# Kernel optimization log

Measured on AMD Instinct MI355X. Metric: run time of the kernel, lower is better.

The kernel has to match this reference:

```python
import jax, jax.numpy as jnp
import numpy as np

B, S, H, NH = 4, 2048, 256, 8
EPS = 1e-5


def setup_inputs() -> dict:
    key = jax.random.key(0)
    ks = jax.random.split(key, 12)
    p = lambda k, shape: (jax.random.normal(k, shape, jnp.float32) * 0.02)
    return {
        "x": jax.random.normal(ks[0], (B, S, H), jnp.float32),
        "lengths": jax.random.randint(ks[1], (B,), 0, S).astype(jnp.int32),
        "atten_in": jnp.zeros((1,), jnp.float32),
        "Wq": p(ks[2], (H, H)), "bq": jnp.zeros((H,), jnp.float32),
        "Wk": p(ks[3], (H, H)), "bk": jnp.zeros((H,), jnp.float32),
        "Wv": p(ks[4], (H, H)), "bv": jnp.zeros((H,), jnp.float32),
        "W1": p(ks[5], (H, H)), "b1": jnp.zeros((H,), jnp.float32),
        "W2": p(ks[6], (H, H)), "b2": jnp.zeros((H,), jnp.float32),
        "g1": jnp.ones((H,), jnp.float32), "beta1": jnp.zeros((H,), jnp.float32),
        "g2": jnp.ones((H,), jnp.float32), "beta2": jnp.zeros((H,), jnp.float32),
    }


def _layer_norm(x, g, b):
    mu = x.mean(-1, keepdims=True)
    var = ((x - mu) ** 2).mean(-1, keepdims=True)
    return (x - mu) / jnp.sqrt(var + EPS) * g + b


def reference(x, lengths, atten_in, Wq, bq, Wk, bk, Wv, bv, W1, b1, W2, b2, g1, beta1, g2, beta2):
    Bx, Sx, Hx = x.shape
    hd = Hx // NH
    # QKV projections, split heads -> [B, NH, S, hd]
    q = (x @ Wq + bq).reshape(Bx, Sx, NH, hd).transpose(0, 2, 1, 3)
    k = (x @ Wk + bk).reshape(Bx, Sx, NH, hd).transpose(0, 2, 1, 3)
    v = (x @ Wv + bv).reshape(Bx, Sx, NH, hd).transpose(0, 2, 1, 3)
    # NOTE: original scales by sqrt(hidden_size), not sqrt(head_dim)
    scores = jnp.einsum('bhqd,bhkd->bhqk', q, k) / np.sqrt(Hx).astype(np.float32)
    pos = jnp.arange(Sx)
    causal = pos[:, None] >= pos[None, :]                     # [S, S]
    row_ok = pos[None, :] < lengths[:, None]                  # [B, S]: mask query rows >= length
    head_ok = jnp.arange(NH)[None, :] < lengths[:, None]      # [B, NH]: original loop masks heads >= length
    mask = causal[None, None] & row_ok[:, None, :, None] & head_ok[:, :, None, None]
    neg = jnp.finfo(scores.dtype).min
    logits = jnp.where(mask, scores, neg)
    atten = jax.nn.softmax(logits, axis=-1)
    # original: masked_fill((atten > 0) == False, 0) -> fully masked rows (NaN in torch) become 0
    atten = jnp.where(mask, atten, 0.0)
    row_valid = mask.any(-1, keepdims=True)
    atten = jnp.where(row_valid, atten, 0.0)
    out = jnp.einsum('bhqk,bhkd->bhqd', atten, v).transpose(0, 2, 1, 3).reshape(Bx, Sx, Hx)
    atten_mean = atten.mean(axis=1)  # [B, S, S], detached in original
    out_1 = x + out  # dropout p=0 / eval mode -> identity
    out_1_norm = _layer_norm(out_1, g1, beta1)
    ff = jax.nn.gelu(out_1_norm @ W1 + b1, approximate=False) @ W2 + b2
    y_prim = _layer_norm(out_1_norm + ff, g2, beta2)
    return (y_prim, lengths, atten_mean)
```

## Files before the change

kernel.cpp:

```cpp
#include <hip/hip_runtime.h>
#include <math.h>

#define BB 4
#define SS 2048
#define HH 256
#define NHH 8
#define EPSV 1e-5f
#define NC 8
#define CHW (SS/NC)
#define NCO 4
#define QPRE 0.09016844005556021f

#if __has_builtin(__builtin_amdgcn_exp2f)
#define EXP2F(x) __builtin_amdgcn_exp2f(x)
#else
#define EXP2F(x) __expf((x) * 0.6931471805599453f)
#endif

typedef unsigned short ushortT;
typedef __attribute__((ext_vector_type(8))) short bf16x8;
typedef __attribute__((ext_vector_type(4))) float f32x4;

__device__ inline ushortT f2bf(float f) {
    union { float f; unsigned int u; } x; x.f = f;
    unsigned int r = x.u + 0x7FFFu + ((x.u >> 16) & 1u);
    return (ushortT)(r >> 16);
}
__device__ inline ushortT f2bf_rz(float f) {
    union { float f; unsigned int u; } x; x.f = f;
    return (ushortT)(x.u >> 16);
}
__device__ inline float bf2f(ushortT u) {
    union { unsigned int i; float f; } x; x.i = ((unsigned int)u) << 16;
    return x.f;
}

__global__ __launch_bounds__(256) void prep(const float* __restrict__ x,
        ushortT* __restrict__ xb, const int* __restrict__ L,
        float* __restrict__ out_len,
        const float* __restrict__ Wa, const float* __restrict__ Wb,
        const float* __restrict__ Wc, const float* __restrict__ Wd,
        const float* __restrict__ We, ushortT* __restrict__ Wtb) {
    const int bid = blockIdx.x;
    if (bid < 1024) {
        const int i = (bid * 256 + threadIdx.x) << 3;
        float4 v0 = *(const float4*)(x + i);
        float4 v1 = *(const float4*)(x + i + 4);
        bf16x8 o;
        o[0] = (short)f2bf(v0.x); o[1] = (short)f2bf(v0.y);
        o[2] = (short)f2bf(v0.z); o[3] = (short)f2bf(v0.w);
        o[4] = (short)f2bf(v1.x); o[5] = (short)f2bf(v1.y);
        o[6] = (short)f2bf(v1.z); o[7] = (short)f2bf(v1.w);
        *(bf16x8*)(xb + i) = o;
        if (bid == 0 && threadIdx.x < BB) out_len[threadIdx.x] = (float)L[threadIdx.x];
        return;
    }
    const int wb = bid - 1024;
    const int z = wb >> 6;
    const int rem = wb & 63;
    const int k0 = (rem >> 3) << 5, n0 = (rem & 7) << 5;
    const float* W = (z == 0) ? Wa : (z == 1) ? Wb : (z == 2) ? Wc : (z == 3) ? Wd : We;
    __shared__ float tile[32][33];
    const int t = threadIdx.x;
    const int r = t >> 3, c4 = (t & 7) << 2;
    float4 v = *(const float4*)(W + (size_t)(k0 + r) * HH + n0 + c4);
    tile[r][c4+0] = v.x; tile[r][c4+1] = v.y; tile[r][c4+2] = v.z; tile[r][c4+3] = v.w;
    __syncthreads();
    ushort4 o;
    o.x = f2bf(tile[c4+0][r]); o.y = f2bf(tile[c4+1][r]);
    o.z = f2bf(tile[c4+2][r]); o.w = f2bf(tile[c4+3][r]);
    *(ushort4*)(Wtb + (size_t)z * 65536 + (size_t)(n0 + r) * HH + k0 + c4) = o;
}

__global__ __launch_bounds__(256) void gemm_qkv(const ushortT* __restrict__ A,
        const ushortT* __restrict__ Wtb,
        const float* __restrict__ bq, const float* __restrict__ bk,
        const float* __restrict__ bv,
        ushortT* __restrict__ Qb, ushortT* __restrict__ Kb,
        ushortT* __restrict__ Vt) {
    __shared__ ushortT As[64][264];
    __shared__ ushortT Ws[64][264];
    const int wsel = blockIdx.y >> 2;
    const int n0 = (blockIdx.y & 3) << 6;
    const ushortT* Wt = Wtb + (size_t)wsel * 65536;
    const float* bias = (wsel == 0) ? bq : (wsel == 1) ? bk : bv;
    const int tid = threadIdx.x;
    const int m0 = blockIdx.x << 6;
    #pragma unroll
    for (int t = 0; t < 8; ++t) {
        const int f = t * 256 + tid;
        const int r = f >> 5;
        const int cc = (f & 31) << 3;
        *(bf16x8*)&As[r][cc] = *(const bf16x8*)(A + (size_t)(m0 + r) * HH + cc);
        *(bf16x8*)&Ws[r][cc] = *(const bf16x8*)(Wt + (size_t)(n0 + r) * HH + cc);
    }
    __syncthreads();
    const int w = tid >> 6, lane = tid & 63;
    const int lg = lane >> 4, lc = lane & 15;
    const int wr = (w & 1) << 5, wc = (w >> 1) << 5;
    f32x4 acc[2][2];
    const f32x4 z4 = {0.f, 0.f, 0.f, 0.f};
    acc[0][0] = z4; acc[0][1] = z4; acc[1][0] = z4; acc[1][1] = z4;
    #pragma unroll
    for (int k0 = 0; k0 < 256; k0 += 32) {
        bf16x8 a0 = *(const bf16x8*)&As[wr + lc][k0 + lg*8];
        bf16x8 a1 = *(const bf16x8*)&As[wr + 16 + lc][k0 + lg*8];
        bf16x8 b0 = *(const bf16x8*)&Ws[wc + lc][k0 + lg*8];
        bf16x8 b1 = *(const bf16x8*)&Ws[wc + 16 + lc][k0 + lg*8];
        acc[0][0] = __builtin_amdgcn_mfma_f32_16x16x32_bf16(a0, b0, acc[0][0], 0, 0, 0);
        acc[0][1] = __builtin_amdgcn_mfma_f32_16x16x32_bf16(a0, b1, acc[0][1], 0, 0, 0);
        acc[1][0] = __builtin_amdgcn_mfma_f32_16x16x32_bf16(a1, b0, acc[1][0], 0, 0, 0);
        acc[1][1] = __builtin_amdgcn_mfma_f32_16x16x32_bf16(a1, b1, acc[1][1], 0, 0, 0);
    }
    ushortT* Out = (wsel == 0) ? Qb : Kb;
    #pragma unroll
    for (int RH = 0; RH < 2; ++RH)
        #pragma unroll
        for (int CH = 0; CH < 2; ++CH) {
            const int col = n0 + wc + CH*16 + lc;
            const float bvv = bias[col];
            float v[4];
            #pragma unroll
            for (int r = 0; r < 4; ++r) {
                v[r] = acc[RH][CH][r] + bvv;
                if (wsel == 0) v[r] *= QPRE;
            }
            if (wsel < 2) {
                #pragma unroll
                for (int r = 0; r < 4; ++r) {
                    const int row = m0 + wr + RH*16 + lg*4 + r;
                    Out[(size_t)row * HH + col] = f2bf(v[r]);
                }
            } else {
                const int row0 = m0 + wr + RH*16 + lg*4;
                const int bidx = row0 >> 11, s0 = row0 & (SS - 1);
                ushort4 o;
                o.x = f2bf(v[0]); o.y = f2bf(v[1]); o.z = f2bf(v[2]); o.w = f2bf(v[3]);
                *(ushort4*)(Vt + ((size_t)(bidx * HH + col)) * SS + s0) = o;
            }
        }
}

template<int MODE>
__global__ __launch_bounds__(256) void gemm_mfma(const ushortT* __restrict__ A,
        const ushortT* __restrict__ Wt, const float* __restrict__ bias,
        void* __restrict__ Cv) {
    __shared__ ushortT As[64][264];
    __shared__ ushortT Ws[64][264];
    const int tid = threadIdx.x;
    const int m0 = blockIdx.x << 6;
    const int n0 = blockIdx.y << 6;
    #pragma unroll
    for (int t = 0; t < 8; ++t) {
        const int f = t * 256 + tid;
        const int r = f >> 5;
        const int cc = (f & 31) << 3;
        *(bf16x8*)&As[r][cc] = *(const bf16x8*)(A + (size_t)(m0 + r) * HH + cc);
        *(bf16x8*)&Ws[r][cc] = *(const bf16x8*)(Wt + (size_t)(n0 + r) * HH + cc);
    }
    __syncthreads();
    const int w = tid >> 6, lane = tid & 63;
    const int lg = lane >> 4, lc = lane & 15;
    const int wr = (w & 1) << 5, wc = (w >> 1) << 5;
    f32x4 acc[2][2];
    const f32x4 z4 = {0.f, 0.f, 0.f, 0.f};
    acc[0][0] = z4; acc[0][1] = z4; acc[1][0] = z4; acc[1][1] = z4;
    #pragma unroll
    for (int k0 = 0; k0 < 256; k0 += 32) {
        bf16x8 a0 = *(const bf16x8*)&As[wr + lc][k0 + lg*8];
        bf16x8 a1 = *(const bf16x8*)&As[wr + 16 + lc][k0 + lg*8];
        bf16x8 b0 = *(const bf16x8*)&Ws[wc + lc][k0 + lg*8];
        bf16x8 b1 = *(const bf16x8*)&Ws[wc + 16 + lc][k0 + lg*8];
        acc[0][0] = __builtin_amdgcn_mfma_f32_16x16x32_bf16(a0, b0, acc[0][0], 0, 0, 0);
        acc[0][1] = __builtin_amdgcn_mfma_f32_16x16x32_bf16(a0, b1, acc[0][1], 0, 0, 0);
        acc[1][0] = __builtin_amdgcn_mfma_f32_16x16x32_bf16(a1, b0, acc[1][0], 0, 0, 0);
        acc[1][1] = __builtin_amdgcn_mfma_f32_16x16x32_bf16(a1, b1, acc[1][1], 0, 0, 0);
    }
    #pragma unroll
    for (int RH = 0; RH < 2; ++RH)
        #pragma unroll
        for (int CH = 0; CH < 2; ++CH) {
            const int col = n0 + wc + CH*16 + lc;
            const float bv = bias[col];
            #pragma unroll
            for (int r = 0; r < 4; ++r) {
                const int row = m0 + wr + RH*16 + lg*4 + r;
                float v = acc[RH][CH][r] + bv;
                if (MODE == 2) v = 0.5f * v * (1.0f + erff(v * 0.70710678118f));
                if (MODE == 0) ((float*)Cv)[(size_t)row * HH + col] = v;
                else           ((ushortT*)Cv)[(size_t)row * HH + col] = f2bf(v);
            }
        }
}

__global__ __launch_bounds__(512) void attn_sums(const ushortT* __restrict__ Qb,
        const ushortT* __restrict__ Kb, const int* __restrict__ lengths,
        float* __restrict__ Psum) {
    const int b = blockIdx.z, c = blockIdx.y;
    const int i0 = (63 - blockIdx.x) << 5;
    const int len = lengths[b];
    const int jmax = min(i0 + 31, len - 1);
    const int jstart = c * CHW;
    if (i0 >= len || jstart > jmax) return;
    const int tid = threadIdx.x;
    const int w = tid >> 6, lane = tid & 63;
    const int lg = lane >> 4, lc = lane & 15;
    bf16x8 qf[2];
    #pragma unroll
    for (int RH = 0; RH < 2; ++RH)
        qf[RH] = *(const bf16x8*)(Qb + ((size_t)(b * SS + i0 + RH*16 + lc)) * HH + w*32 + lg*8);
    const f32x4 z4 = {0.f, 0.f, 0.f, 0.f};
    float lsum[2][4] = {};
    const int jend = min(jstart + CHW - 32, (jmax >> 5) << 5);
    bf16x8 kf0 = *(const bf16x8*)(Kb + ((size_t)(b * SS + jstart + lc)) * HH + w*32 + lg*8);
    bf16x8 kf1 = *(const bf16x8*)(Kb + ((size_t)(b * SS + jstart + 16 + lc)) * HH + w*32 + lg*8);
    for (int j0 = jstart; j0 <= jend; j0 += 32) {
        bf16x8 ck0 = kf0, ck1 = kf1;
        if (j0 + 32 <= jend) {
            kf0 = *(const bf16x8*)(Kb + ((size_t)(b * SS + j0 + 32 + lc)) * HH + w*32 + lg*8);
            kf1 = *(const bf16x8*)(Kb + ((size_t)(b * SS + j0 + 48 + lc)) * HH + w*32 + lg*8);
        }
        f32x4 s[2][2];
        #pragma unroll
        for (int RH = 0; RH < 2; ++RH) {
            s[RH][0] = __builtin_amdgcn_mfma_f32_16x16x32_bf16(qf[RH], ck0, z4, 0, 0, 0);
            s[RH][1] = __builtin_amdgcn_mfma_f32_16x16x32_bf16(qf[RH], ck1, z4, 0, 0, 0);
        }
        if (j0 < i0) {
            #pragma unroll
            for (int RH = 0; RH < 2; ++RH)
                #pragma unroll
                for (int r = 0; r < 4; ++r)
                    #pragma unroll
                    for (int CH = 0; CH < 2; ++CH)
                        lsum[RH][r] += EXP2F(s[RH][CH][r]);
        } else {
            #pragma unroll
            for (int RH = 0; RH < 2; ++RH)
                #pragma unroll
                for (int r = 0; r < 4; ++r) {
                    const int row = i0 + RH*16 + lg*4 + r;
                    #pragma unroll
                    for (int CH = 0; CH < 2; ++CH) {
                        const int j = j0 + CH*16 + lc;
                        lsum[RH][r] += (j <= row) ? EXP2F(s[RH][CH][r]) : 0.f;
                    }
                }
        }
    }
    #pragma unroll
    for (int RH = 0; RH < 2; ++RH)
        #pragma unroll
        for (int r = 0; r < 4; ++r) {
            float v = lsum[RH][r];
            v += __shfl_xor(v, 1); v += __shfl_xor(v, 2);
            v += __shfl_xor(v, 4); v += __shfl_xor(v, 8);
            if (lc == 0)
                Psum[((size_t)(c * BB + b) * NHH + w) * SS + i0 + RH*16 + lg*4 + r] = v;
        }
}

__global__ __launch_bounds__(512) void attn_pv(const ushortT* __restrict__ Qb,
        const ushortT* __restrict__ Kb, const ushortT* __restrict__ Vt,
        const int* __restrict__ lengths, const float* __restrict__ Psum,
        ushortT* __restrict__ OPart, float* __restrict__ out_mean) {
    __shared__ __align__(16) ushortT Pb[2][NHH][32][40];
    __shared__ float invS[NHH][32];
    const int b = blockIdx.z, cg = blockIdx.y;
    const int i0 = (63 - blockIdx.x) << 5;
    const int len = lengths[b];
    const int tid = threadIdx.x;
    const int mr = tid >> 4, mc = (tid & 15) << 1;
    float* meanrow = out_mean + ((size_t)(b * SS + i0 + mr)) * SS + mc;
    const int T = (i0 < len) ? ((min(i0 + 31, len - 1) >> 5) + 1) : 0;
    for (int t = T + ((cg - T) & (NCO - 1)); t < 64; t += NCO)
        *(float2*)(meanrow + (t << 5)) = make_float2(0.f, 0.f);
    const int q = T >> 2, r = T & (NCO - 1);
    const int t0 = cg * q + min(cg, r);
    const int t1 = t0 + q + (cg < r ? 1 : 0);
    if (t0 >= t1) return;
    if (tid < NHH * 32) {
        const int hh = tid >> 5, row = i0 + (tid & 31);
        float rv = 0.f;
        if (row < len && hh < len) {
            float s = 0.f;
            const int ncv = (row >> 8) + 1;
            for (int c2 = 0; c2 < ncv; ++c2)
                s += Psum[((size_t)(c2 * BB + b) * NHH + hh) * SS + row];
            rv = (s > 0.f) ? 1.0f / s : 0.f;
        }
        invS[hh][tid & 31] = rv;
    }
    __syncthreads();
    const int w = tid >> 6, lane = tid & 63;
    const int lg = lane >> 4, lc = lane & 15;
    bf16x8 qf[2];
    #pragma unroll
    for (int RH = 0; RH < 2; ++RH)
        qf[RH] = *(const bf16x8*)(Qb + ((size_t)(b * SS + i0 + RH*16 + lc)) * HH + w*32 + lg*8);
    float invv[2][4];
    #pragma unroll
    for (int RH = 0; RH < 2; ++RH)
        #pragma unroll
        for (int r2 = 0; r2 < 4; ++r2)
            invv[RH][r2] = invS[w][RH*16 + lg*4 + r2];
    float invh8[NHH];
    #pragma unroll
    for (int hh = 0; hh < NHH; ++hh)
        invh8[hh] = invS[hh][mr] * 0.125f;
    const f32x4 z4 = {0.f, 0.f, 0.f, 0.f};
    f32x4 O[2][2];
    O[0][0] = z4; O[0][1] = z4; O[1][0] = z4; O[1][1] = z4;
    const int jstart = t0 << 5;
    bf16x8 kf0 = *(const bf16x8*)(Kb + ((size_t)(b * SS + jstart + lc)) * HH + w*32 + lg*8);
    bf16x8 kf1 = *(const bf16x8*)(Kb + ((size_t)(b * SS + jstart + 16 + lc)) * HH + w*32 + lg*8);
    bf16x8 vf0 = *(const bf16x8*)(Vt + ((size_t)(b * HH + w*32 + lc)) * SS + jstart + lg*8);
    bf16x8 vf1 = *(const bf16x8*)(Vt + ((size_t)(b * HH + w*32 + 16 + lc)) * SS + jstart + lg*8);
    int par = 0;
    for (int t = t0; t < t1; ++t) {
        const int j0 = t << 5;
        bf16x8 ck0 = kf0, ck1 = kf1, cv0 = vf0, cv1 = vf1;
        if (t + 1 < t1) {
            kf0 = *(const bf16x8*)(Kb + ((size_t)(b * SS + j0 + 32 + lc)) * HH + w*32 + lg*8);
            kf1 = *(const bf16x8*)(Kb + ((size_t)(b * SS + j0 + 48 + lc)) * HH + w*32 + lg*8);
            vf0 = *(const bf16x8*)(Vt + ((size_t)(b * HH + w*32 + lc)) * SS + j0 + 32 + lg*8);
            vf1 = *(const bf16x8*)(Vt + ((size_t)(b * HH + w*32 + 16 + lc)) * SS + j0 + 32 + lg*8);
        }
        f32x4 s[2][2];
        #pragma unroll
        for (int RH = 0; RH < 2; ++RH) {
            s[RH][0] = __builtin_amdgcn_mfma_f32_16x16x32_bf16(qf[RH], ck0, z4, 0, 0, 0);
            s[RH][1] = __builtin_amdgcn_mfma_f32_16x16x32_bf16(qf[RH], ck1, z4, 0, 0, 0);
        }
        if (j0 < i0) {
            #pragma unroll
            for (int RH = 0; RH < 2; ++RH)
                #pragma unroll
                for (int CH = 0; CH < 2; ++CH)
                    #pragma unroll
                    for (int r2 = 0; r2 < 4; ++r2)
                        Pb[par][w][RH*16 + lg*4 + r2][CH*16 + lc] =
                            f2bf_rz(EXP2F(s[RH][CH][r2]));
        } else {
            #pragma unroll
            for (int RH = 0; RH < 2; ++RH)
                #pragma unroll
                for (int CH = 0; CH < 2; ++CH)
                    #pragma unroll
                    for (int r2 = 0; r2 < 4; ++r2) {
                        const int row = i0 + RH*16 + lg*4 + r2;
                        const int j = j0 + CH*16 + lc;
                        Pb[par][w][RH*16 + lg*4 + r2][CH*16 + lc] =
                            (j <= row) ? f2bf_rz(EXP2F(s[RH][CH][r2])) : (ushortT)0;
                    }
        }
        #pragma unroll
        for (int RH = 0; RH < 2; ++RH) {
            bf16x8 pa = *(const bf16x8*)&Pb[par][w][RH*16 + lc][lg*8];
            O[RH][0] = __builtin_amdgcn_mfma_f32_16x16x32_bf16(pa, cv0, O[RH][0], 0, 0, 0);
            O[RH][1] = __builtin_amdgcn_mfma_f32_16x16x32_bf16(pa, cv1, O[RH][1], 0, 0, 0);
        }
        __syncthreads();
        float m0 = 0.f, m1 = 0.f;
        #pragma unroll
        for (int ww = 0; ww < NHH; ++ww) {
            ushort2 t2 = *(const ushort2*)&Pb[par][ww][mr][mc];
            m0 += bf2f(t2.x) * invh8[ww]; m1 += bf2f(t2.y) * invh8[ww];
        }
        *(float2*)(meanrow + j0) = make_float2(m0, m1);
        par ^= 1;
    }
    ushortT* op = OPart + (size_t)cg * ((size_t)BB * SS * HH);
    #pragma unroll
    for (int RH = 0; RH < 2; ++RH)
        #pragma unroll
        for (int DH = 0; DH < 2; ++DH)
            #pragma unroll
            for (int r2 = 0; r2 < 4; ++r2)
                op[((size_t)(b * SS + i0 + RH*16 + lg*4 + r2)) * HH + w*32 + DH*16 + lc] =
                    f2bf(O[RH][DH][r2] * invv[RH][r2]);
}

__global__ __launch_bounds__(256) void add_ln_attn(const float* __restrict__ x,
        const ushortT* __restrict__ OPart, const int* __restrict__ lengths,
        const float* __restrict__ g, const float* __restrict__ beta,
        float* __restrict__ out, ushortT* __restrict__ outb) {
    const int row = blockIdx.x;
    const int c = threadIdx.x;
    const int i = row & (SS - 1);
    const int len = lengths[row >> 11];
    const size_t base = (size_t)row * 256;
    float v = x[base + c];
    if (i < len) {
        const int ncv = min(NCO, (i >> 5) + 1);
        for (int cc = 0; cc < ncv; ++cc)
            v += bf2f(OPart[(size_t)cc * ((size_t)BB * SS * HH) + base + c]);
    }
    __shared__ float red[8];
    float s = v;
    #pragma unroll
    for (int o = 32; o; o >>= 1) s += __shfl_down(s, o, 64);
    const int wid = c >> 6, lane = c & 63;
    if (lane == 0) red[wid] = s;
    __syncthreads();
    float mu = (red[0] + red[1] + red[2] + red[3]) * 0.00390625f;
    float d = v - mu;
    float q = d * d;
    #pragma unroll
    for (int o = 32; o; o >>= 1) q += __shfl_down(q, o, 64);
    if (lane == 0) red[4 + wid] = q;
    __syncthreads();
    float var = (red[4] + red[5] + red[6] + red[7]) * 0.00390625f;
    float res = d * rsqrtf(var + EPSV) * g[c] + beta[c];
    out[base + c] = res;
    outb[base + c] = f2bf(res);
}

__global__ __launch_bounds__(256) void add_ln(const float* __restrict__ A,
        const float* __restrict__ Bv, const float* __restrict__ g,
        const float* __restrict__ beta, float* __restrict__ out) {
    const int row = blockIdx.x;
    const int c = threadIdx.x;
    const size_t base = (size_t)row * 256;
    float v = A[base + c] + Bv[base + c];
    __shared__ float red[8];
    float s = v;
    #pragma unroll
    for (int o = 32; o; o >>= 1) s += __shfl_down(s, o, 64);
    const int wid = c >> 6, lane = c & 63;
    if (lane == 0) red[wid] = s;
    __syncthreads();
    float mu = (red[0] + red[1] + red[2] + red[3]) * 0.00390625f;
    float d = v - mu;
    float q = d * d;
    #pragma unroll
    for (int o = 32; o; o >>= 1) q += __shfl_down(q, o, 64);
    if (lane == 0) red[4 + wid] = q;
    __syncthreads();
    float var = (red[4] + red[5] + red[6] + red[7]) * 0.00390625f;
    out[base + c] = d * rsqrtf(var + EPSV) * g[c] + beta[c];
}

extern "C" void kernel_launch(void* const* d_in, const int* in_sizes, int n_in,
                              void* d_out, int out_size, void* d_ws, size_t ws_size,
                              hipStream_t stream) {
    const float* x   = (const float*)d_in[0];
    const int* lengths = (const int*)d_in[1];
    const float* Wq  = (const float*)d_in[3];
    const float* bq  = (const float*)d_in[4];
    const float* Wk  = (const float*)d_in[5];
    const float* bk  = (const float*)d_in[6];
    const float* Wv  = (const float*)d_in[7];
    const float* bv  = (const float*)d_in[8];
    const float* W1  = (const float*)d_in[9];
    const float* b1  = (const float*)d_in[10];
    const float* W2  = (const float*)d_in[11];
    const float* b2  = (const float*)d_in[12];
    const float* g1  = (const float*)d_in[13];
    const float* be1 = (const float*)d_in[14];
    const float* g2  = (const float*)d_in[15];
    const float* be2 = (const float*)d_in[16];
    float* out = (float*)d_out;
    float* ws  = (float*)d_ws;

    const size_t NELT = (size_t)BB * SS * HH;
    const size_t M1 = 1024 * 1024;

    ushortT* xb  = (ushortT*)ws;
    float*   Psum = ws;
    ushortT* Qbf = (ushortT*)(ws + M1);
    ushortT* Kbf = (ushortT*)(ws + 2 * M1);
    ushortT* Vtb = (ushortT*)(ws + 3 * M1);
    float*   X1N  = ws + 4 * M1;
    ushortT* Wtb = (ushortT*)(ws + 6 * M1);
    ushortT* OPart = (ushortT*)(ws + 7 * M1);
    ushortT* X1Nb = (ushortT*)ws;
    ushortT* F1b  = (ushortT*)(ws + M1);
    float*   F2   = ws + 2 * M1;

    float* out_y    = out;
    float* out_len  = out + NELT;
    float* out_mean = out + NELT + 4;

    prep<<<1344, 256, 0, stream>>>(x, xb, lengths, out_len, Wq, Wk, Wv, W1, W2, Wtb);
    gemm_qkv<<<dim3(128, 12), 256, 0, stream>>>(xb, Wtb, bq, bk, bv, Qbf, Kbf, Vtb);
    attn_sums<<<dim3(64, NC, 4), 512, 0, stream>>>(Qbf, Kbf, lengths, Psum);
    attn_pv<<<dim3(64, NCO, 4), 512, 0, stream>>>(Qbf, Kbf, Vtb, lengths, Psum, OPart, out_mean);
    add_ln_attn<<<8192, 256, 0, stream>>>(x, OPart, lengths, g1, be1, X1N, X1Nb);
    gemm_mfma<2><<<dim3(128, 4), 256, 0, stream>>>(X1Nb, Wtb + 3 * 65536, b1, (void*)F1b);
    gemm_mfma<0><<<dim3(128, 4), 256, 0, stream>>>(F1b,  Wtb + 4 * 65536, b2, (void*)F2);
    add_ln<<<8192, 256, 0, stream>>>(X1N, F2, g2, be2, out_y);
}
```

Measured before the change: 104.4 us.

## Widen attention-mean and output stores in attn_pv via batched tiles and LDS staging

The zero-fill of the masked region of atten_mean becomes contiguous float4 row segments split evenly across the column-group blocks, replacing strided float2 stores. The per-tile mean reduction now runs once per pair of 32-column tiles, so it syncs half as often and writes float4 per thread. The bf16 partial output is staged through LDS and written as 16-byte row-contiguous vectors instead of scattered 2-byte stores. This adds an extra barrier per pair and reuses the Pb buffer for staging, so correctness depends on the parity and sync logic being right.

```diff
diff --git a/kernel.cpp b/kernel.cpp
--- a/kernel.cpp
+++ b/kernel.cpp
@@ -270,11 +270,22 @@
     const int i0 = (63 - blockIdx.x) << 5;
     const int len = lengths[b];
     const int tid = threadIdx.x;
-    const int mr = tid >> 4, mc = (tid & 15) << 1;
-    float* meanrow = out_mean + ((size_t)(b * SS + i0 + mr)) * SS + mc;
+    const int mr = tid >> 4;
+    const int w = tid >> 6, lane = tid & 63;
+    const int lg = lane >> 4, lc = lane & 15;
     const int T = (i0 < len) ? ((min(i0 + 31, len - 1) >> 5) + 1) : 0;
-    for (int t = T + ((cg - T) & (NCO - 1)); t < 64; t += NCO)
-        *(float2*)(meanrow + (t << 5)) = make_float2(0.f, 0.f);
+    {
+        const int zc0 = T << 5;
+        const int zq = (SS - zc0) >> 2;
+        const int c0 = zc0 + cg * zq;
+        const int c1 = c0 + zq;
+        #pragma unroll
+        for (int rr = 0; rr < 4; ++rr) {
+            float* mrow0 = out_mean + ((size_t)(b * SS + i0 + w * 4 + rr)) * SS;
+            for (int cc2 = c0 + (lane << 2); cc2 < c1; cc2 += 256)
+                *(float4*)(mrow0 + cc2) = make_float4(0.f, 0.f, 0.f, 0.f);
+        }
+    }
     const int q = T >> 2, r = T & (NCO - 1);
     const int t0 = cg * q + min(cg, r);
     const int t1 = t0 + q + (cg < r ? 1 : 0);
@@ -292,8 +303,6 @@
         invS[hh][tid & 31] = rv;
     }
     __syncthreads();
-    const int w = tid >> 6, lane = tid & 63;
-    const int lg = lane >> 4, lc = lane & 15;
     bf16x8 qf[2];
     #pragma unroll
     for (int RH = 0; RH < 2; ++RH)
@@ -360,25 +369,49 @@
             O[RH][0] = __builtin_amdgcn_mfma_f32_16x16x32_bf16(pa, cv0, O[RH][0], 0, 0, 0);
             O[RH][1] = __builtin_amdgcn_mfma_f32_16x16x32_bf16(pa, cv1, O[RH][1], 0, 0, 0);
         }
-        __syncthreads();
-        float m0 = 0.f, m1 = 0.f;
-        #pragma unroll
-        for (int ww = 0; ww < NHH; ++ww) {
-            ushort2 t2 = *(const ushort2*)&Pb[par][ww][mr][mc];
-            m0 += bf2f(t2.x) * invh8[ww]; m1 += bf2f(t2.y) * invh8[ww];
-        }
-        *(float2*)(meanrow + j0) = make_float2(m0, m1);
-        par ^= 1;
-    }
+        if (par == 1 || t == t1 - 1) {
+            __syncthreads();
+            const int nc = (par + 1) << 5;
+            const int base = (t - par) << 5;
+            const int cb = (tid & 15) << 2;
+            if (cb < nc) {
+                const int sel = cb >> 5, coff = cb & 31;
+                float m0 = 0.f, m1 = 0.f, m2 = 0.f, m3 = 0.f;
+                #pragma unroll
+                for (int ww = 0; ww < NHH; ++ww) {
+                    ushort4 t4 = *(const ushort4*)&Pb[sel][ww][mr][coff];
+                    m0 += bf2f(t4.x) * invh8[ww];
+                    m1 += bf2f(t4.y) * invh8[ww];
+                    m2 += bf2f(t4.z) * invh8[ww];
+                    m3 += bf2f(t4.w) * invh8[ww];
+                }
+                *(float4*)(out_mean + ((size_t)(b * SS + i0 + mr)) * SS + base + cb)
+                    = make_float4(m0, m1, m2, m3);
+            }
+            __syncthreads();
+            par = 0;
+        } else {
+            par = 1;
+        }
+    }
+    ushortT* OLs = &Pb[0][0][0][0];
+    #pragma unroll
+    for (int RH = 0; RH < 2; ++RH)
+        #pragma unroll
+        for (int DH = 0; DH < 2; ++DH)
+            #pragma unroll
+            for (int r2 = 0; r2 < 4; ++r2)
+                OLs[(RH*16 + lg*4 + r2) * 264 + w*32 + DH*16 + lc] =
+                    f2bf(O[RH][DH][r2] * invv[RH][r2]);
+    __syncthreads();
     ushortT* op = OPart + (size_t)cg * ((size_t)BB * SS * HH);
     #pragma unroll
-    for (int RH = 0; RH < 2; ++RH)
-        #pragma unroll
-        for (int DH = 0; DH < 2; ++DH)
-            #pragma unroll
-            for (int r2 = 0; r2 < 4; ++r2)
-                op[((size_t)(b * SS + i0 + RH*16 + lg*4 + r2)) * HH + w*32 + DH*16 + lc] =
-                    f2bf(O[RH][DH][r2] * invv[RH][r2]);
+    for (int rr = 0; rr < 4; rr += 2) {
+        const int row = w*4 + rr + (lane >> 5);
+        const int c8 = (lane & 31) << 3;
+        *(bf16x8*)(op + ((size_t)(b * SS + i0 + row)) * HH + c8) =
+            *(const bf16x8*)&OLs[row * 264 + c8];
+    }
 }
 
 __global__ __launch_bounds__(256) void add_ln_attn(const float* __restrict__ x,
```

Measured after the change: 110.2 us. 5.6% more time.

## Split attention-mean computation out of attn_pv into a separate kernel

Applied to the files above, without the earlier changes.

Moves the head-averaged attention matrix out of attn_pv into a new attn_mean kernel. attn_mean recomputes QK^T for all heads per 32x32 tile and accumulates normalized exp values in registers. attn_pv no longer needs double-buffered LDS, the per-tile __syncthreads, or the cross-wave mean reduction, and the mean work is spread over more blocks (NC=8 column chunks). The cost is a second full QK^T plus exp pass and an extra kernel launch, and the mean is now computed from fp32 exps rather than bf16-rounded probabilities.

```diff
diff --git a/kernel.cpp b/kernel.cpp
--- a/kernel.cpp
+++ b/kernel.cpp
@@ -260,21 +260,108 @@
         }
 }
 
+__global__ __launch_bounds__(512) void attn_mean(const ushortT* __restrict__ Qb,
+        const ushortT* __restrict__ Kb, const int* __restrict__ lengths,
+        const float* __restrict__ Psum, float* __restrict__ out_mean) {
+    __shared__ float invS[NHH][32];
+    const int b = blockIdx.z, c = blockIdx.y;
+    const int i0 = (63 - blockIdx.x) << 5;
+    const int len = lengths[b];
+    const int tid = threadIdx.x;
+    const int w = tid >> 6, lane = tid & 63;
+    const int lg = lane >> 4, lc = lane & 15;
+    const int T = (i0 < len) ? ((min(i0 + 31, len - 1) >> 5) + 1) : 0;
+    {
+        const int zs = max(T * 32 - c * 256, 0);
+        if (zs < 256) {
+            #pragma unroll
+            for (int rr = 0; rr < 4; ++rr) {
+                float* mrow = out_mean + ((size_t)(b * SS + i0 + w * 4 + rr)) * SS + c * 256;
+                const int col = zs + (lane << 2);
+                if (col < 256)
+                    *(float4*)(mrow + col) = make_float4(0.f, 0.f, 0.f, 0.f);
+            }
+        }
+    }
+    if (c * 8 >= T) return;
+    if (tid < NHH * 32) {
+        const int hh = tid >> 5, row = i0 + (tid & 31);
+        float rv = 0.f;
+        if (row < len && hh < len) {
+            float s = 0.f;
+            const int ncv = (row >> 8) + 1;
+            for (int c2 = 0; c2 < ncv; ++c2)
+                s += Psum[((size_t)(c2 * BB + b) * NHH + hh) * SS + row];
+            rv = (s > 0.f) ? 0.125f / s : 0.f;
+        }
+        invS[hh][tid & 31] = rv;
+    }
+    __syncthreads();
+    const int tw = c * 8 + w;
+    if (tw >= T) return;
+    const int j0 = tw << 5;
+    const f32x4 z4 = {0.f, 0.f, 0.f, 0.f};
+    float macc[2][2][4] = {};
+    #pragma unroll
+    for (int h = 0; h < NHH; ++h) {
+        bf16x8 q0 = *(const bf16x8*)(Qb + ((size_t)(b * SS + i0 + lc)) * HH + h*32 + lg*8);
+        bf16x8 q1 = *(const bf16x8*)(Qb + ((size_t)(b * SS + i0 + 16 + lc)) * HH + h*32 + lg*8);
+        bf16x8 k0 = *(const bf16x8*)(Kb + ((size_t)(b * SS + j0 + lc)) * HH + h*32 + lg*8);
+        bf16x8 k1 = *(const bf16x8*)(Kb + ((size_t)(b * SS + j0 + 16 + lc)) * HH + h*32 + lg*8);
+        f32x4 s[2][2];
+        s[0][0] = __builtin_amdgcn_mfma_f32_16x16x32_bf16(q0, k0, z4, 0, 0, 0);
+        s[0][1] = __builtin_amdgcn_mfma_f32_16x16x32_bf16(q0, k1, z4, 0, 0, 0);
+        s[1][0] = __builtin_amdgcn_mfma_f32_16x16x32_bf16(q1, k0, z4, 0, 0, 0);
+        s[1][1] = __builtin_amdgcn_mfma_f32_16x16x32_bf16(q1, k1, z4, 0, 0, 0);
+        float invr[2][4];
+        #pragma unroll
+        for (int RH = 0; RH < 2; ++RH)
+            #pragma unroll
+            for (int r = 0; r < 4; ++r)
+                invr[RH][r] = invS[h][RH*16 + lg*4 + r];
+        if (j0 < i0) {
+            #pragma unroll
+            for (int RH = 0; RH < 2; ++RH)
+                #pragma unroll
+                for (int CH = 0; CH < 2; ++CH)
+                    #pragma unroll
+                    for (int r = 0; r < 4; ++r)
+                        macc[RH][CH][r] += EXP2F(s[RH][CH][r]) * invr[RH][r];
+        } else {
+            #pragma unroll
+            for (int RH = 0; RH < 2; ++RH)
+                #pragma unroll
+                for (int CH = 0; CH < 2; ++CH)
+                    #pragma unroll
+                    for (int r = 0; r < 4; ++r) {
+                        const int row = i0 + RH*16 + lg*4 + r;
+                        const int j = j0 + CH*16 + lc;
+                        if (j <= row)
+                            macc[RH][CH][r] += EXP2F(s[RH][CH][r]) * invr[RH][r];
+                    }
+        }
+    }
+    #pragma unroll
+    for (int RH = 0; RH < 2; ++RH)
+        #pragma unroll
+        for (int CH = 0; CH < 2; ++CH)
+            #pragma unroll
+            for (int r = 0; r < 4; ++r)
+                out_mean[((size_t)(b * SS + i0 + RH*16 + lg*4 + r)) * SS + j0 + CH*16 + lc]
+                    = macc[RH][CH][r];
+}
+
 __global__ __launch_bounds__(512) void attn_pv(const ushortT* __restrict__ Qb,
         const ushortT* __restrict__ Kb, const ushortT* __restrict__ Vt,
         const int* __restrict__ lengths, const float* __restrict__ Psum,
-        ushortT* __restrict__ OPart, float* __restrict__ out_mean) {
-    __shared__ __align__(16) ushortT Pb[2][NHH][32][40];
+        ushortT* __restrict__ OPart) {
+    __shared__ __align__(16) ushortT Pb[NHH][32][40];
     __shared__ float invS[NHH][32];
     const int b = blockIdx.z, cg = blockIdx.y;
     const int i0 = (63 - blockIdx.x) << 5;
     const int len = lengths[b];
     const int tid = threadIdx.x;
-    const int mr = tid >> 4, mc = (tid & 15) << 1;
-    float* meanrow = out_mean + ((size_t)(b * SS + i0 + mr)) * SS + mc;
     const int T = (i0 < len) ? ((min(i0 + 31, len - 1) >> 5) + 1) : 0;
-    for (int t = T + ((cg - T) & (NCO - 1)); t < 64; t += NCO)
-        *(float2*)(meanrow + (t << 5)) = make_float2(0.f, 0.f);
     const int q = T >> 2, r = T & (NCO - 1);
     const int t0 = cg * q + min(cg, r);
     const int t1 = t0 + q + (cg < r ? 1 : 0);
@@ -304,10 +391,6 @@
         #pragma unroll
         for (int r2 = 0; r2 < 4; ++r2)
             invv[RH][r2] = invS[w][RH*16 + lg*4 + r2];
-    float invh8[NHH];
-    #pragma unroll
-    for (int hh = 0; hh < NHH; ++hh)
-        invh8[hh] = invS[hh][mr] * 0.125f;
     const f32x4 z4 = {0.f, 0.f, 0.f, 0.f};
     f32x4 O[2][2];
     O[0][0] = z4; O[0][1] = z4; O[1][0] = z4; O[1][1] = z4;
@@ -316,7 +399,6 @@
     bf16x8 kf1 = *(const bf16x8*)(Kb + ((size_t)(b * SS + jstart + 16 + lc)) * HH + w*32 + lg*8);
     bf16x8 vf0 = *(const bf16x8*)(Vt + ((size_t)(b * HH + w*32 + lc)) * SS + jstart + lg*8);
     bf16x8 vf1 = *(const bf16x8*)(Vt + ((size_t)(b * HH + w*32 + 16 + lc)) * SS + jstart + lg*8);
-    int par = 0;
     for (int t = t0; t < t1; ++t) {
         const int j0 = t << 5;
         bf16x8 ck0 = kf0, ck1 = kf1, cv0 = vf0, cv1 = vf1;
@@ -339,7 +421,7 @@
                 for (int CH = 0; CH < 2; ++CH)
                     #pragma unroll
                     for (int r2 = 0; r2 < 4; ++r2)
-                        Pb[par][w][RH*16 + lg*4 + r2][CH*16 + lc] =
+                        Pb[w][RH*16 + lg*4 + r2][CH*16 + lc] =
                             f2bf_rz(EXP2F(s[RH][CH][r2]));
         } else {
             #pragma unroll
@@ -350,25 +432,16 @@
                     for (int r2 = 0; r2 < 4; ++r2) {
                         const int row = i0 + RH*16 + lg*4 + r2;
                         const int j = j0 + CH*16 + lc;
-                        Pb[par][w][RH*16 + lg*4 + r2][CH*16 + lc] =
+                        Pb[w][RH*16 + lg*4 + r2][CH*16 + lc] =
                             (j <= row) ? f2bf_rz(EXP2F(s[RH][CH][r2])) : (ushortT)0;
                     }
         }
         #pragma unroll
         for (int RH = 0; RH < 2; ++RH) {
-            bf16x8 pa = *(const bf16x8*)&Pb[par][w][RH*16 + lc][lg*8];
+            bf16x8 pa = *(const bf16x8*)&Pb[w][RH*16 + lc][lg*8];
             O[RH][0] = __builtin_amdgcn_mfma_f32_16x16x32_bf16(pa, cv0, O[RH][0], 0, 0, 0);
             O[RH][1] = __builtin_amdgcn_mfma_f32_16x16x32_bf16(pa, cv1, O[RH][1], 0, 0, 0);
         }
-        __syncthreads();
-        float m0 = 0.f, m1 = 0.f;
-        #pragma unroll
-        for (int ww = 0; ww < NHH; ++ww) {
-            ushort2 t2 = *(const ushort2*)&Pb[par][ww][mr][mc];
-            m0 += bf2f(t2.x) * invh8[ww]; m1 += bf2f(t2.y) * invh8[ww];
-        }
-        *(float2*)(meanrow + j0) = make_float2(m0, m1);
-        par ^= 1;
     }
     ushortT* op = OPart + (size_t)cg * ((size_t)BB * SS * HH);
     #pragma unroll
@@ -485,7 +558,8 @@
     prep<<<1344, 256, 0, stream>>>(x, xb, lengths, out_len, Wq, Wk, Wv, W1, W2, Wtb);
     gemm_qkv<<<dim3(128, 12), 256, 0, stream>>>(xb, Wtb, bq, bk, bv, Qbf, Kbf, Vtb);
     attn_sums<<<dim3(64, NC, 4), 512, 0, stream>>>(Qbf, Kbf, lengths, Psum);
-    attn_pv<<<dim3(64, NCO, 4), 512, 0, stream>>>(Qbf, Kbf, Vtb, lengths, Psum, OPart, out_mean);
+    attn_pv<<<dim3(64, NCO, 4), 512, 0, stream>>>(Qbf, Kbf, Vtb, lengths, Psum, OPart);
+    attn_mean<<<dim3(64, NC, 4), 512, 0, stream>>>(Qbf, Kbf, lengths, Psum, out_mean);
     add_ln_attn<<<8192, 256, 0, stream>>>(x, OPart, lengths, g1, be1, X1N, X1Nb);
     gemm_mfma<2><<<dim3(128, 4), 256, 0, stream>>>(X1Nb, Wtb + 3 * 65536, b1, (void*)F1b);
     gemm_mfma<0><<<dim3(128, 4), 256, 0, stream>>>(F1b,  Wtb + 4 * 65536, b2, (void*)F2);
```

New measurement: 124.9 us. 19.6% more time.
